# Optimization experiments

Hardware: AMD Instinct MI355X
Metric: run time of the kernel (lower is better)

## Reference

```python
import jax, jax.numpy as jnp
import numpy as np

N, E, D, L = 100000, 500000, 128, 5
NUM_ATOM_FEATS, ATOM_VOCAB = 9, 120
NUM_BOND_FEATS, BOND_VOCAB = 3, 8
BN_EPS = 1e-5


def setup_inputs() -> dict:
    key = jax.random.key(0)
    ks = jax.random.split(key, 16)
    inp = {
        "x": jax.random.randint(ks[0], (N, NUM_ATOM_FEATS), 0, ATOM_VOCAB),
        "edge_index": jax.random.randint(ks[1], (2, E), 0, N),
        "edge_attr": jax.random.randint(ks[2], (E, NUM_BOND_FEATS), 0, BOND_VOCAB),
        "edge_weight": jax.random.uniform(ks[3], (E,), dtype=jnp.float32),
        # parameters
        "atom_emb": jax.random.normal(ks[4], (NUM_ATOM_FEATS, ATOM_VOCAB, D), dtype=jnp.float32) * 0.02,
        "bond_emb": jax.random.normal(ks[5], (L, NUM_BOND_FEATS, BOND_VOCAB, D), dtype=jnp.float32) * 0.02,
        "eps": jnp.zeros((L,), dtype=jnp.float32),
        "W1": jax.random.normal(ks[6], (L, D, 2 * D), dtype=jnp.float32) / np.sqrt(D),
        "b1": jnp.zeros((L, 2 * D), dtype=jnp.float32),
        "g1": jnp.ones((L, 2 * D), dtype=jnp.float32),
        "bt1": jnp.zeros((L, 2 * D), dtype=jnp.float32),
        "W2": jax.random.normal(ks[7], (L, 2 * D, D), dtype=jnp.float32) / np.sqrt(2 * D),
        "b2": jnp.zeros((L, D), dtype=jnp.float32),
        "g_out": jnp.ones((L, D), dtype=jnp.float32),
        "bt_out": jnp.zeros((L, D), dtype=jnp.float32),
    }
    return inp


def _batchnorm(h, g, b):
    # training-mode BN over node axis, biased variance (matches torch BN normalization)
    mu = jnp.mean(h, axis=0)
    var = jnp.mean((h - mu) ** 2, axis=0)
    return g * (h - mu) * jax.lax.rsqrt(var + BN_EPS) + b


def reference(x, edge_index, edge_attr, edge_weight,
              atom_emb, bond_emb, eps, W1, b1, g1, bt1, W2, b2, g_out, bt_out):
    # AtomEncoder: sum per-column embedding lookups -> [N, D]
    h = atom_emb[jnp.arange(NUM_ATOM_FEATS)[None, :], x].sum(axis=1)
    src, dst = edge_index[0], edge_index[1]
    ew = edge_weight[:, None]
    for l in range(L):
        # BondEncoder for layer l -> [E, D]
        e = bond_emb[l][jnp.arange(NUM_BOND_FEATS)[None, :], edge_attr].sum(axis=1)
        # message: relu(x_j + edge_emb) * edge_weight ; aggregate: scatter-add at dst
        m = jax.nn.relu(h[src] + e) * ew
        agg = jax.ops.segment_sum(m, dst, num_segments=N)
        z = (1.0 + eps[l]) * h + agg
        # GIN MLP: Linear -> BN -> ReLU -> Linear
        z = jax.nn.relu(_batchnorm(z @ W1[l] + b1[l], g1[l], bt1[l])) @ W2[l] + b2[l]
        # outer BatchNorm; dropout is identity in eval mode
        h_new = _batchnorm(z, g_out[l], bt_out[l])
        h = h_new if l == L - 1 else jax.nn.relu(h_new)
    return h
```

## Files before the change

### kernel.cpp

```cpp
#include <hip/hip_runtime.h>
#include <hip/hip_bf16.h>
#include <hip/hip_fp16.h>

#define NN 100000
#define EE 500000
#define NP 100096

typedef _Float16 f16;
typedef __attribute__((ext_vector_type(8))) _Float16 f16x8;
typedef __attribute__((ext_vector_type(4))) _Float16 f16x4;
typedef __attribute__((ext_vector_type(4))) float f32x4;

__global__ __launch_bounds__(256) void prep_kernel(const float* __restrict__ W1,
                                                   const float* __restrict__ W2,
                                                   const float* __restrict__ bemb,
                                                   f16* __restrict__ w1f,
                                                   f16* __restrict__ w2f,
                                                   f16* __restrict__ bembf) {
  int gid = blockIdx.x * 256 + threadIdx.x;
  if (gid < 163840) {
    int l = gid / 32768; int rem = gid % 32768;
    int k = rem / 256;   int n = rem % 256;
    int ctg = n >> 4, m = n & 15;
    int c = k >> 5, q = (k >> 3) & 3, e = k & 7;
    int lane = q * 16 + m;
    w1f[l * 32768 + ((ctg * 4 + c) * 64 + lane) * 8 + e] = (f16)W1[gid];
  } else if (gid < 327680) {
    int g = gid - 163840;
    int l = g / 32768; int rem = g % 32768;
    int k = rem / 128; int n = rem % 128;
    int ctg = n >> 4, m = n & 15;
    int c = k >> 5, q = (k >> 3) & 3, e = k & 7;
    int lane = q * 16 + m;
    w2f[l * 32768 + ((ctg * 8 + c) * 64 + lane) * 8 + e] = (f16)W2[g];
  } else if (gid < 343040) {
    int g = gid - 327680;
    bembf[g] = (f16)bemb[g];
  }
}

__global__ __launch_bounds__(256) void zero_deg_kernel(int* __restrict__ deg) {
  int i = blockIdx.x * 256 + threadIdx.x;
  if (i < NN) deg[i] = 0;
}

__global__ __launch_bounds__(256) void hist_kernel(const int* __restrict__ ei, int* __restrict__ deg) {
  int e = blockIdx.x * 256 + threadIdx.x;
  if (e < EE) atomicAdd(&deg[ei[EE + e]], 1);
}

__global__ __launch_bounds__(256) void scan1_kernel(const int* __restrict__ deg,
                                                    int* __restrict__ offs,
                                                    int* __restrict__ bsum) {
  __shared__ int sh[256];
  int b = blockIdx.x, t = threadIdx.x;
  int base = b * 1024 + t * 4;
  int v[4];
  int s = 0;
#pragma unroll
  for (int i = 0; i < 4; ++i) { v[i] = (base + i < NN) ? deg[base + i] : 0; s += v[i]; }
  sh[t] = s;
  __syncthreads();
  for (int off = 1; off < 256; off <<= 1) {
    int x = (t >= off) ? sh[t - off] : 0;
    __syncthreads();
    sh[t] += x;
    __syncthreads();
  }
  int excl = sh[t] - s;
  if (t == 255) bsum[b] = sh[255];
  int run = excl;
#pragma unroll
  for (int i = 0; i < 4; ++i) {
    if (base + i < NN) offs[base + i] = run;
    run += v[i];
  }
}

__global__ void scan2_kernel(int* __restrict__ bsum, int nb) {
  if (threadIdx.x == 0 && blockIdx.x == 0) {
    int run = 0;
    for (int i = 0; i < nb; ++i) { int v = bsum[i]; bsum[i] = run; run += v; }
  }
}

__global__ __launch_bounds__(256) void scan3_kernel(int* __restrict__ offs,
                                                    const int* __restrict__ bsum,
                                                    int* __restrict__ cursor) {
  int i = blockIdx.x * 256 + threadIdx.x;
  if (i < NN) {
    int v = offs[i] + bsum[i >> 10];
    offs[i] = v;
    cursor[i] = v;
  } else if (i == NN) {
    offs[NN] = EE;
  }
}

__global__ __launch_bounds__(256) void scatter_kernel(const int* __restrict__ ei,
                                                      const int* __restrict__ ea,
                                                      const float* __restrict__ ew,
                                                      int* __restrict__ cursor,
                                                      int* __restrict__ pk,
                                                      float* __restrict__ wsrt) {
  int e = blockIdx.x * 256 + threadIdx.x;
  if (e >= EE) return;
  int dst = ei[EE + e];
  int pos = atomicAdd(&cursor[dst], 1);
  int src = ei[e];
  int a0 = ea[e * 3 + 0], a1 = ea[e * 3 + 1], a2 = ea[e * 3 + 2];
  pk[pos] = src | (a0 << 17) | (a1 << 20) | (a2 << 23);
  wsrt[pos] = ew[e];
}

__global__ __launch_bounds__(256) void zero_slices_kernel(float* __restrict__ p) {
  int i = blockIdx.x * 256 + threadIdx.x;
  *(float4*)(p + i * 4) = float4{0.f, 0.f, 0.f, 0.f};
}

__global__ __launch_bounds__(256) void atom_kernel(const int* __restrict__ x,
                                                   const float* __restrict__ aemb,
                                                   f16* __restrict__ hf) {
  int gid = blockIdx.x * 256 + threadIdx.x;
  int n = gid >> 5, qq = gid & 31;
  if (n >= NN) return;
  float4 s = {0.f, 0.f, 0.f, 0.f};
#pragma unroll
  for (int f = 0; f < 9; ++f) {
    int xi = x[n * 9 + f];
    float4 v = *(const float4*)(aemb + (f * 120 + xi) * 128 + qq * 4);
    s.x += v.x; s.y += v.y; s.z += v.z; s.w += v.w;
  }
  f16x4 o;
  o[0] = (f16)s.x; o[1] = (f16)s.y; o[2] = (f16)s.z; o[3] = (f16)s.w;
  *(f16x4*)(hf + (long)n * 128 + qq * 4) = o;
}

__global__ __launch_bounds__(256) void edge_agg_kernel(const int* __restrict__ offs,
                                                       const int* __restrict__ pk,
                                                       const float* __restrict__ wsrt,
                                                       const f16* __restrict__ bembf,
                                                       const float* __restrict__ eps, int l,
                                                       const f16* __restrict__ hf,
                                                       f16* __restrict__ zb) {
  int gid = blockIdx.x * 256 + threadIdx.x;
  int n = gid >> 4, d0 = (gid & 15) * 8;
  if (n >= NN) {
    f16x8 z = {0, 0, 0, 0, 0, 0, 0, 0};
    *(f16x8*)(zb + (long)n * 128 + d0) = z;
    return;
  }
  int s0 = offs[n], s1 = offs[n + 1];
  float e1 = 1.f + eps[l];
  f16x8 hn = *(const f16x8*)(hf + (long)n * 128 + d0);
  float acc[8];
#pragma unroll
  for (int i = 0; i < 8; ++i) acc[i] = e1 * (float)hn[i];
  for (int e = s0; e < s1; ++e) {
    int p = pk[e];
    float w = wsrt[e];
    int src = p & 131071;
    f16x8 b0 = *(const f16x8*)(bembf + (((p >> 17) & 7)) * 128 + d0);
    f16x8 b1 = *(const f16x8*)(bembf + (8 + ((p >> 20) & 7)) * 128 + d0);
    f16x8 b2 = *(const f16x8*)(bembf + (16 + ((p >> 23) & 7)) * 128 + d0);
    f16x8 hs = *(const f16x8*)(hf + (long)src * 128 + d0);
    f16x8 sm = hs + b0 + b1 + b2;
#pragma unroll
    for (int i = 0; i < 8; ++i) {
      float sv = (float)sm[i];
      acc[i] += fmaxf(sv, 0.f) * w;
    }
  }
  f16x8 o;
#pragma unroll
  for (int i = 0; i < 8; ++i) o[i] = (f16)acc[i];
  *(f16x8*)(zb + (long)n * 128 + d0) = o;
}

__global__ __launch_bounds__(256) void gemm1_kernel(const f16* __restrict__ zb,
                                                    const f16* __restrict__ w1f,
                                                    f16* __restrict__ t1f,
                                                    float* __restrict__ sum1s,
                                                    float* __restrict__ sq1s) {
  __shared__ __align__(16) char ldsraw[17408];
  const int tid = threadIdx.x;
  const int lane = tid & 63, w = tid >> 6;
  const int wr = w >> 1, wc = w & 1;
  const int m = lane & 15, q = lane >> 4;
  const int rbase = blockIdx.x * 64;
  const int cb = blockIdx.y;
  const int slice = blockIdx.x & 15;

  f16x8 B[4][4];
#pragma unroll
  for (int ct = 0; ct < 4; ++ct)
#pragma unroll
    for (int c = 0; c < 4; ++c)
      B[ct][c] = *(const f16x8*)(w1f + (((cb * 8 + wc * 4 + ct) * 4 + c) * 64 + lane) * 8);

  {
    f16x8 st[4];
    const int tofs = tid * 16;
#pragma unroll
    for (int j = 0; j < 4; ++j)
      st[j] = *(const f16x8*)(zb + (long)rbase * 128 + (tofs + j * 4096) / 2);
#pragma unroll
    for (int j = 0; j < 4; ++j) {
      int ofs = tofs + j * 4096;
      int row = ofs >> 8, colb = ofs & 255;
      *(f16x8*)(ldsraw + row * 256 + (colb ^ ((row & 7) << 4))) = st[j];
    }
  }
  __syncthreads();

  f16x8 A[2][4];
#pragma unroll
  for (int rt = 0; rt < 2; ++rt) {
    int row = wr * 32 + rt * 16 + m;
    int rs = row * 256, sw = (row & 7) << 4;
#pragma unroll
    for (int c = 0; c < 4; ++c) {
      int colb = c * 64 + q * 16;
      A[rt][c] = *(const f16x8*)(ldsraw + rs + (colb ^ sw));
    }
  }

  f32x4 acc[2][4];
  const f32x4 zf = {0.f, 0.f, 0.f, 0.f};
#pragma unroll
  for (int a = 0; a < 2; ++a)
#pragma unroll
    for (int b = 0; b < 4; ++b) acc[a][b] = zf;

#pragma unroll
  for (int c = 0; c < 4; ++c)
#pragma unroll
    for (int rt = 0; rt < 2; ++rt)
#pragma unroll
      for (int ct = 0; ct < 4; ++ct)
        acc[rt][ct] = __builtin_amdgcn_mfma_f32_16x16x32_f16(A[rt][c], B[ct][c], acc[rt][ct], 0, 0, 0);

  __syncthreads();
  f16 (*sh)[136] = (f16(*)[136])ldsraw;

#pragma unroll
  for (int ct = 0; ct < 4; ++ct) {
    int lc = wc * 64 + ct * 16 + m;
    int gc = cb * 128 + lc;
    float s = 0.f, s2 = 0.f;
#pragma unroll
    for (int rt = 0; rt < 2; ++rt) {
      int lr = wr * 32 + rt * 16 + q * 4;
#pragma unroll
      for (int i = 0; i < 4; ++i) {
        float v = acc[rt][ct][i];
        s += v; s2 += v * v;
        sh[lr + i][lc] = (f16)v;
      }
    }
    s  += __shfl_xor(s, 16);  s  += __shfl_xor(s, 32);
    s2 += __shfl_xor(s2, 16); s2 += __shfl_xor(s2, 32);
    if (q == 0) {
      unsafeAtomicAdd(&sum1s[slice * 256 + gc], s);
      unsafeAtomicAdd(&sq1s[slice * 256 + gc], s2);
    }
  }
  __syncthreads();
  const int colc = tid & 15, r0 = tid >> 4;
#pragma unroll
  for (int j = 0; j < 4; ++j) {
    int r = j * 16 + r0;
    f16x8 v = *(const f16x8*)(&sh[r][colc * 8]);
    *(f16x8*)(t1f + (long)(rbase + r) * 256 + cb * 128 + colc * 8) = v;
  }
}

__global__ void stats_kernel(float* __restrict__ sums, float* __restrict__ sqs,
                             const float* __restrict__ g, const float* __restrict__ bt,
                             float* __restrict__ scale, float* __restrict__ shift, int C) {
  int j = blockIdx.x * blockDim.x + threadIdx.x;
  if (j >= C) return;
  float s = 0.f, s2 = 0.f;
#pragma unroll
  for (int k = 0; k < 16; ++k) {
    s += sums[k * C + j]; s2 += sqs[k * C + j];
    sums[k * C + j] = 0.f; sqs[k * C + j] = 0.f;
  }
  float mu = s * (1.f / NN);
  float var = s2 * (1.f / NN) - mu * mu;
  var = fmaxf(var, 0.f);
  float is = rsqrtf(var + 1e-5f);
  float sc = g[j] * is;
  scale[j] = sc;
  shift[j] = bt[j] - mu * sc;
}

__global__ __launch_bounds__(256) void gemm2_kernel(const f16* __restrict__ a1,
                                                    const f16* __restrict__ w2f,
                                                    const float* __restrict__ scale1,
                                                    const float* __restrict__ shift1,
                                                    f16* __restrict__ zb,
                                                    float* __restrict__ sum2s,
                                                    float* __restrict__ sq2s) {
  __shared__ __align__(16) char ldsraw[32768];
  const int tid = threadIdx.x;
  const int lane = tid & 63, w = tid >> 6;
  const int wr = w >> 1, wc = w & 1;
  const int m = lane & 15, q = lane >> 4;
  const int rbase = blockIdx.x * 64;
  const int slice = blockIdx.x & 15;

  {
    f16x8 st[8];
    const int tofs = tid * 16;
#pragma unroll
    for (int j = 0; j < 8; ++j)
      st[j] = *(const f16x8*)(a1 + (long)rbase * 256 + (tofs + j * 4096) / 2);
#pragma unroll
    for (int j = 0; j < 8; ++j) {
      int ofs = tofs + j * 4096;
      int row = ofs >> 9, colb = ofs & 511;
      int k0 = colb >> 1;
      float4 sa = *(const float4*)(scale1 + k0);
      float4 sb = *(const float4*)(scale1 + k0 + 4);
      float4 ha = *(const float4*)(shift1 + k0);
      float4 hb = *(const float4*)(shift1 + k0 + 4);
      f16x8 u = st[j], o;
      o[0] = (f16)fmaxf((float)u[0] * sa.x + ha.x, 0.f);
      o[1] = (f16)fmaxf((float)u[1] * sa.y + ha.y, 0.f);
      o[2] = (f16)fmaxf((float)u[2] * sa.z + ha.z, 0.f);
      o[3] = (f16)fmaxf((float)u[3] * sa.w + ha.w, 0.f);
      o[4] = (f16)fmaxf((float)u[4] * sb.x + hb.x, 0.f);
      o[5] = (f16)fmaxf((float)u[5] * sb.y + hb.y, 0.f);
      o[6] = (f16)fmaxf((float)u[6] * sb.z + hb.z, 0.f);
      o[7] = (f16)fmaxf((float)u[7] * sb.w + hb.w, 0.f);
      *(f16x8*)(ldsraw + row * 512 + (colb ^ ((row & 7) << 4))) = o;
    }
  }
  __syncthreads();

  f32x4 acc[2][4];
  const f32x4 zf = {0.f, 0.f, 0.f, 0.f};
#pragma unroll
  for (int a = 0; a < 2; ++a)
#pragma unroll
    for (int b = 0; b < 4; ++b) acc[a][b] = zf;

#pragma unroll
  for (int hh = 0; hh < 2; ++hh) {
    f16x8 A[2][4], B[4][4];
#pragma unroll
    for (int rt = 0; rt < 2; ++rt) {
      int row = wr * 32 + rt * 16 + m;
      int rs = row * 512, sw = (row & 7) << 4;
#pragma unroll
      for (int c = 0; c < 4; ++c) {
        int colb = (hh * 4 + c) * 64 + q * 16;
        A[rt][c] = *(const f16x8*)(ldsraw + rs + (colb ^ sw));
      }
    }
#pragma unroll
    for (int ct = 0; ct < 4; ++ct)
#pragma unroll
      for (int c = 0; c < 4; ++c)
        B[ct][c] = *(const f16x8*)(w2f + (((wc * 4 + ct) * 8 + hh * 4 + c) * 64 + lane) * 8);
#pragma unroll
    for (int c = 0; c < 4; ++c)
#pragma unroll
      for (int rt = 0; rt < 2; ++rt)
#pragma unroll
        for (int ct = 0; ct < 4; ++ct)
          acc[rt][ct] = __builtin_amdgcn_mfma_f32_16x16x32_f16(A[rt][c], B[ct][c], acc[rt][ct], 0, 0, 0);
  }

  __syncthreads();
  f16 (*sh)[136] = (f16(*)[136])ldsraw;

#pragma unroll
  for (int ct = 0; ct < 4; ++ct) {
    int gc = wc * 64 + ct * 16 + m;
    float s = 0.f, s2 = 0.f;
#pragma unroll
    for (int rt = 0; rt < 2; ++rt) {
      int grow = rbase + wr * 32 + rt * 16 + q * 4;
      int lr = wr * 32 + rt * 16 + q * 4;
#pragma unroll
      for (int i = 0; i < 4; ++i) {
        float v = acc[rt][ct][i];
        float vv = (grow + i < NN) ? v : 0.f;
        s += vv; s2 += vv * vv;
        sh[lr + i][gc] = (f16)v;
      }
    }
    s  += __shfl_xor(s, 16);  s  += __shfl_xor(s, 32);
    s2 += __shfl_xor(s2, 16); s2 += __shfl_xor(s2, 32);
    if (q == 0) {
      unsafeAtomicAdd(&sum2s[slice * 128 + gc], s);
      unsafeAtomicAdd(&sq2s[slice * 128 + gc], s2);
    }
  }
  __syncthreads();
  const int colc = tid & 15, r0 = tid >> 4;
#pragma unroll
  for (int j = 0; j < 4; ++j) {
    int r = j * 16 + r0;
    f16x8 v = *(const f16x8*)(&sh[r][colc * 8]);
    *(f16x8*)(zb + (long)(rbase + r) * 128 + colc * 8) = v;
  }
}

__global__ __launch_bounds__(256) void apply_kernel(const f16* __restrict__ zb,
                                                    const float* __restrict__ scale2,
                                                    const float* __restrict__ shift2,
                                                    int last,
                                                    f16* __restrict__ hf,
                                                    float* __restrict__ outp) {
  int gid = blockIdx.x * 256 + threadIdx.x;
  int n = gid >> 5, qq = gid & 31;
  if (n >= NN) return;
  f16x4 u = *(const f16x4*)(zb + (long)n * 128 + qq * 4);
  float4 sc = *(const float4*)(scale2 + qq * 4);
  float4 sh = *(const float4*)(shift2 + qq * 4);
  float y0 = (float)u[0] * sc.x + sh.x;
  float y1 = (float)u[1] * sc.y + sh.y;
  float y2 = (float)u[2] * sc.z + sh.z;
  float y3 = (float)u[3] * sc.w + sh.w;
  if (last) {
    float4 o = {y0, y1, y2, y3};
    *(float4*)(outp + (long)n * 128 + qq * 4) = o;
  } else {
    f16x4 o;
    o[0] = (f16)fmaxf(y0, 0.f); o[1] = (f16)fmaxf(y1, 0.f);
    o[2] = (f16)fmaxf(y2, 0.f); o[3] = (f16)fmaxf(y3, 0.f);
    *(f16x4*)(hf + (long)n * 128 + qq * 4) = o;
  }
}

extern "C" void kernel_launch(void* const* d_in, const int* in_sizes, int n_in,
                              void* d_out, int out_size, void* d_ws, size_t ws_size,
                              hipStream_t stream) {
  (void)in_sizes; (void)n_in; (void)out_size; (void)ws_size;
  const int*   x      = (const int*)d_in[0];
  const int*   ei     = (const int*)d_in[1];
  const int*   ea     = (const int*)d_in[2];
  const float* ew     = (const float*)d_in[3];
  const float* aemb   = (const float*)d_in[4];
  const float* bemb   = (const float*)d_in[5];
  const float* eps    = (const float*)d_in[6];
  const float* W1     = (const float*)d_in[7];
  const float* g1     = (const float*)d_in[9];
  const float* bt1    = (const float*)d_in[10];
  const float* W2     = (const float*)d_in[11];
  const float* g_out  = (const float*)d_in[13];
  const float* bt_out = (const float*)d_in[14];

  float* outp = (float*)d_out;

  char* ws = (char*)d_ws;
  f16*   hf    = (f16*)(ws);
  f16*   zb    = (f16*)(ws + 25624576);
  f16*   t1f   = (f16*)(ws + 51249152);
  f16*   w1f   = (f16*)(ws + 102498304);
  f16*   w2f   = (f16*)(ws + 102825984);
  f16*   bembf = (f16*)(ws + 103153664);
  float* ssbuf = (float*)(ws + 103184384);
  float* slices= (float*)(ws + 103187456);
  int*   deg    = (int*)(ws + 103236608);
  int*   offs   = (int*)(ws + 103636608);
  int*   cursor = (int*)(ws + 104036624);
  int*   bsum   = (int*)(ws + 104436624);
  int*   pk     = (int*)(ws + 104437024);
  float* wsrt   = (float*)(ws + 106437024);

  float* scale1 = ssbuf;        float* shift1 = ssbuf + 256;
  float* scale2 = ssbuf + 512;  float* shift2 = ssbuf + 640;
  float* sum1s = slices;
  float* sq1s  = slices + 4096;
  float* sum2s = slices + 8192;
  float* sq2s  = slices + 10240;

  prep_kernel<<<1340, 256, 0, stream>>>(W1, W2, bemb, w1f, w2f, bembf);
  zero_deg_kernel<<<391, 256, 0, stream>>>(deg);
  hist_kernel<<<1954, 256, 0, stream>>>(ei, deg);
  scan1_kernel<<<98, 256, 0, stream>>>(deg, offs, bsum);
  scan2_kernel<<<1, 64, 0, stream>>>(bsum, 98);
  scan3_kernel<<<392, 256, 0, stream>>>(offs, bsum, cursor);
  scatter_kernel<<<1954, 256, 0, stream>>>(ei, ea, ew, cursor, pk, wsrt);
  zero_slices_kernel<<<12, 256, 0, stream>>>(slices);
  atom_kernel<<<12500, 256, 0, stream>>>(x, aemb, hf);

  for (int l = 0; l < 5; ++l) {
    edge_agg_kernel<<<6256, 256, 0, stream>>>(offs, pk, wsrt, bembf + l * 3072, eps, l, hf, zb);
    gemm1_kernel<<<dim3(1564, 2), 256, 0, stream>>>(zb, w1f + l * 32768, t1f, sum1s, sq1s);
    stats_kernel<<<1, 256, 0, stream>>>(sum1s, sq1s, g1 + l * 256, bt1 + l * 256, scale1, shift1, 256);
    gemm2_kernel<<<1564, 256, 0, stream>>>(t1f, w2f + l * 32768, scale1, shift1, zb, sum2s, sq2s);
    stats_kernel<<<1, 128, 0, stream>>>(sum2s, sq2s, g_out + l * 128, bt_out + l * 128, scale2, shift2, 128);
    apply_kernel<<<12500, 256, 0, stream>>>(zb, scale2, shift2, (l == 4) ? 1 : 0, hf, outp);
  }
}
```

Before: 673.5 us.

## Fuse BN stats and outer BN apply into neighbouring kernels, drop stats launches

Removes the separate stats kernels and the per-layer apply kernel. Each consumer block now recomputes the BN scale and shift from the per-slice sums. The outer BN plus ReLU of the previous layer is applied on the fly inside the edge aggregation, to both self and neighbour features. Stat-slice zeroing moves into the first block of later kernels, which relies on stream ordering between launches. This saves a full read/write pass over node features and ten or more launches per layer set, at the cost of extra per-edge FMAs and redundant stat reductions in every block.

```diff
diff --git a/kernel.cpp b/kernel.cpp
--- a/kernel.cpp
+++ b/kernel.cpp
@@ -140,7 +140,7 @@
                                                        const int* __restrict__ pk,
                                                        const float* __restrict__ wsrt,
                                                        const f16* __restrict__ bembf,
-                                                       const float* __restrict__ eps, int l,
+                                                       const float* __restrict__ eps,
                                                        const f16* __restrict__ hf,
                                                        f16* __restrict__ zb) {
   int gid = blockIdx.x * 256 + threadIdx.x;
@@ -151,7 +151,7 @@
     return;
   }
   int s0 = offs[n], s1 = offs[n + 1];
-  float e1 = 1.f + eps[l];
+  float e1 = 1.f + eps[0];
   f16x8 hn = *(const f16x8*)(hf + (long)n * 128 + d0);
   float acc[8];
 #pragma unroll
@@ -177,11 +177,83 @@
   *(f16x8*)(zb + (long)n * 128 + d0) = o;
 }
 
+__global__ __launch_bounds__(256) void edge_agg_bn_kernel(const int* __restrict__ offs,
+                                                          const int* __restrict__ pk,
+                                                          const float* __restrict__ wsrt,
+                                                          const f16* __restrict__ bembf,
+                                                          const float* __restrict__ eps, int l,
+                                                          const f16* __restrict__ t2,
+                                                          const float* __restrict__ sum2s,
+                                                          const float* __restrict__ sq2s,
+                                                          const float* __restrict__ g2,
+                                                          const float* __restrict__ bt2,
+                                                          float* __restrict__ s1z,
+                                                          f16* __restrict__ zb) {
+  __shared__ float sc2[128], sh2[128];
+  const int tid = threadIdx.x;
+  if (tid < 128) {
+    float s = 0.f, s2 = 0.f;
+#pragma unroll
+    for (int k = 0; k < 16; ++k) { s += sum2s[k * 128 + tid]; s2 += sq2s[k * 128 + tid]; }
+    float mu = s * (1.f / NN);
+    float var = fmaxf(s2 * (1.f / NN) - mu * mu, 0.f);
+    float is = rsqrtf(var + 1e-5f);
+    float sc = g2[tid] * is;
+    sc2[tid] = sc;
+    sh2[tid] = bt2[tid] - mu * sc;
+  }
+  if (blockIdx.x == 0) {
+#pragma unroll
+    for (int j = 0; j < 8; ++j)
+      *(float4*)(s1z + (j * 256 + tid) * 4) = float4{0.f, 0.f, 0.f, 0.f};
+  }
+  __syncthreads();
+  int gid = blockIdx.x * 256 + tid;
+  int n = gid >> 4, d0 = (gid & 15) * 8;
+  if (n >= NN) {
+    f16x8 z = {0, 0, 0, 0, 0, 0, 0, 0};
+    *(f16x8*)(zb + (long)n * 128 + d0) = z;
+    return;
+  }
+  float4 svA = *(const float4*)(sc2 + d0), svB = *(const float4*)(sc2 + d0 + 4);
+  float4 shA = *(const float4*)(sh2 + d0), shB = *(const float4*)(sh2 + d0 + 4);
+  float sv[8] = {svA.x, svA.y, svA.z, svA.w, svB.x, svB.y, svB.z, svB.w};
+  float hv[8] = {shA.x, shA.y, shA.z, shA.w, shB.x, shB.y, shB.z, shB.w};
+  int s0 = offs[n], s1 = offs[n + 1];
+  float e1 = 1.f + eps[l];
+  f16x8 hn = *(const f16x8*)(t2 + (long)n * 128 + d0);
+  float acc[8];
+#pragma unroll
+  for (int i = 0; i < 8; ++i)
+    acc[i] = e1 * fmaxf((float)hn[i] * sv[i] + hv[i], 0.f);
+  for (int e = s0; e < s1; ++e) {
+    int p = pk[e];
+    float w = wsrt[e];
+    int src = p & 131071;
+    f16x8 b0 = *(const f16x8*)(bembf + (((p >> 17) & 7)) * 128 + d0);
+    f16x8 b1 = *(const f16x8*)(bembf + (8 + ((p >> 20) & 7)) * 128 + d0);
+    f16x8 b2 = *(const f16x8*)(bembf + (16 + ((p >> 23) & 7)) * 128 + d0);
+    f16x8 hs = *(const f16x8*)(t2 + (long)src * 128 + d0);
+    f16x8 bs = b0 + b1 + b2;
+#pragma unroll
+    for (int i = 0; i < 8; ++i) {
+      float y = fmaxf((float)hs[i] * sv[i] + hv[i], 0.f);
+      float s = y + (float)bs[i];
+      acc[i] += fmaxf(s, 0.f) * w;
+    }
+  }
+  f16x8 o;
+#pragma unroll
+  for (int i = 0; i < 8; ++i) o[i] = (f16)acc[i];
+  *(f16x8*)(zb + (long)n * 128 + d0) = o;
+}
+
 __global__ __launch_bounds__(256) void gemm1_kernel(const f16* __restrict__ zb,
                                                     const f16* __restrict__ w1f,
                                                     f16* __restrict__ t1f,
                                                     float* __restrict__ sum1s,
-                                                    float* __restrict__ sq1s) {
+                                                    float* __restrict__ sq1s,
+                                                    float* __restrict__ s2z) {
   __shared__ __align__(16) char ldsraw[17408];
   const int tid = threadIdx.x;
   const int lane = tid & 63, w = tid >> 6;
@@ -191,6 +263,12 @@
   const int cb = blockIdx.y;
   const int slice = blockIdx.x & 15;
 
+  if (blockIdx.x == 0 && cb == 0) {
+#pragma unroll
+    for (int j = 0; j < 4; ++j)
+      *(float4*)(s2z + (j * 256 + tid) * 4) = float4{0.f, 0.f, 0.f, 0.f};
+  }
+
   f16x8 B[4][4];
 #pragma unroll
   for (int ct = 0; ct < 4; ++ct)
@@ -275,34 +353,18 @@
   }
 }
 
-__global__ void stats_kernel(float* __restrict__ sums, float* __restrict__ sqs,
-                             const float* __restrict__ g, const float* __restrict__ bt,
-                             float* __restrict__ scale, float* __restrict__ shift, int C) {
-  int j = blockIdx.x * blockDim.x + threadIdx.x;
-  if (j >= C) return;
-  float s = 0.f, s2 = 0.f;
-#pragma unroll
-  for (int k = 0; k < 16; ++k) {
-    s += sums[k * C + j]; s2 += sqs[k * C + j];
-    sums[k * C + j] = 0.f; sqs[k * C + j] = 0.f;
-  }
-  float mu = s * (1.f / NN);
-  float var = s2 * (1.f / NN) - mu * mu;
-  var = fmaxf(var, 0.f);
-  float is = rsqrtf(var + 1e-5f);
-  float sc = g[j] * is;
-  scale[j] = sc;
-  shift[j] = bt[j] - mu * sc;
-}
-
 __global__ __launch_bounds__(256) void gemm2_kernel(const f16* __restrict__ a1,
                                                     const f16* __restrict__ w2f,
-                                                    const float* __restrict__ scale1,
-                                                    const float* __restrict__ shift1,
-                                                    f16* __restrict__ zb,
+                                                    const float* __restrict__ sum1s,
+                                                    const float* __restrict__ sq1s,
+                                                    const float* __restrict__ g1,
+                                                    const float* __restrict__ bt1,
+                                                    f16* __restrict__ t2out,
                                                     float* __restrict__ sum2s,
                                                     float* __restrict__ sq2s) {
-  __shared__ __align__(16) char ldsraw[32768];
+  __shared__ __align__(16) char ldsraw[34816];
+  float* sc1 = (float*)(ldsraw + 32768);
+  float* sh1 = (float*)(ldsraw + 33792);
   const int tid = threadIdx.x;
   const int lane = tid & 63, w = tid >> 6;
   const int wr = w >> 1, wc = w & 1;
@@ -310,21 +372,35 @@
   const int rbase = blockIdx.x * 64;
   const int slice = blockIdx.x & 15;
 
+  f16x8 st[8];
+  const int tofs = tid * 16;
+#pragma unroll
+  for (int j = 0; j < 8; ++j)
+    st[j] = *(const f16x8*)(a1 + (long)rbase * 256 + (tofs + j * 4096) / 2);
+
   {
-    f16x8 st[8];
-    const int tofs = tid * 16;
-#pragma unroll
-    for (int j = 0; j < 8; ++j)
-      st[j] = *(const f16x8*)(a1 + (long)rbase * 256 + (tofs + j * 4096) / 2);
+    float s = 0.f, s2 = 0.f;
+#pragma unroll
+    for (int k = 0; k < 16; ++k) { s += sum1s[k * 256 + tid]; s2 += sq1s[k * 256 + tid]; }
+    float mu = s * (1.f / NN);
+    float var = fmaxf(s2 * (1.f / NN) - mu * mu, 0.f);
+    float is = rsqrtf(var + 1e-5f);
+    float sc = g1[tid] * is;
+    sc1[tid] = sc;
+    sh1[tid] = bt1[tid] - mu * sc;
+  }
+  __syncthreads();
+
+  {
+    const int k0 = (tid & 31) * 8;
+    float4 sa = *(const float4*)(sc1 + k0);
+    float4 sb = *(const float4*)(sc1 + k0 + 4);
+    float4 ha = *(const float4*)(sh1 + k0);
+    float4 hb = *(const float4*)(sh1 + k0 + 4);
 #pragma unroll
     for (int j = 0; j < 8; ++j) {
       int ofs = tofs + j * 4096;
       int row = ofs >> 9, colb = ofs & 511;
-      int k0 = colb >> 1;
-      float4 sa = *(const float4*)(scale1 + k0);
-      float4 sb = *(const float4*)(scale1 + k0 + 4);
-      float4 ha = *(const float4*)(shift1 + k0);
-      float4 hb = *(const float4*)(shift1 + k0 + 4);
       f16x8 u = st[j], o;
       o[0] = (f16)fmaxf((float)u[0] * sa.x + ha.x, 0.f);
       o[1] = (f16)fmaxf((float)u[1] * sa.y + ha.y, 0.f);
@@ -405,34 +481,48 @@
   for (int j = 0; j < 4; ++j) {
     int r = j * 16 + r0;
     f16x8 v = *(const f16x8*)(&sh[r][colc * 8]);
-    *(f16x8*)(zb + (long)(rbase + r) * 128 + colc * 8) = v;
-  }
-}
-
-__global__ __launch_bounds__(256) void apply_kernel(const f16* __restrict__ zb,
-                                                    const float* __restrict__ scale2,
-                                                    const float* __restrict__ shift2,
-                                                    int last,
-                                                    f16* __restrict__ hf,
+    *(f16x8*)(t2out + (long)(rbase + r) * 128 + colc * 8) = v;
+  }
+}
+
+__global__ __launch_bounds__(256) void apply_kernel(const f16* __restrict__ t2,
+                                                    const float* __restrict__ sum2s,
+                                                    const float* __restrict__ sq2s,
+                                                    const float* __restrict__ g2,
+                                                    const float* __restrict__ bt2,
                                                     float* __restrict__ outp) {
-  int gid = blockIdx.x * 256 + threadIdx.x;
-  int n = gid >> 5, qq = gid & 31;
-  if (n >= NN) return;
-  f16x4 u = *(const f16x4*)(zb + (long)n * 128 + qq * 4);
-  float4 sc = *(const float4*)(scale2 + qq * 4);
-  float4 sh = *(const float4*)(shift2 + qq * 4);
-  float y0 = (float)u[0] * sc.x + sh.x;
-  float y1 = (float)u[1] * sc.y + sh.y;
-  float y2 = (float)u[2] * sc.z + sh.z;
-  float y3 = (float)u[3] * sc.w + sh.w;
-  if (last) {
-    float4 o = {y0, y1, y2, y3};
-    *(float4*)(outp + (long)n * 128 + qq * 4) = o;
-  } else {
-    f16x4 o;
-    o[0] = (f16)fmaxf(y0, 0.f); o[1] = (f16)fmaxf(y1, 0.f);
-    o[2] = (f16)fmaxf(y2, 0.f); o[3] = (f16)fmaxf(y3, 0.f);
-    *(f16x4*)(hf + (long)n * 128 + qq * 4) = o;
+  __shared__ float sc2[128], sh2[128];
+  const int tid = threadIdx.x;
+  if (tid < 128) {
+    float s = 0.f, s2 = 0.f;
+#pragma unroll
+    for (int k = 0; k < 16; ++k) { s += sum2s[k * 128 + tid]; s2 += sq2s[k * 128 + tid]; }
+    float mu = s * (1.f / NN);
+    float var = fmaxf(s2 * (1.f / NN) - mu * mu, 0.f);
+    float is = rsqrtf(var + 1e-5f);
+    float sc = g2[tid] * is;
+    sc2[tid] = sc;
+    sh2[tid] = bt2[tid] - mu * sc;
+  }
+  __syncthreads();
+  const int rbase = blockIdx.x * 64;
+#pragma unroll
+  for (int k = 0; k < 4; ++k) {
+    int ci = tid + k * 256;
+    int r = ci >> 4, c8 = ci & 15;
+    int row = rbase + r;
+    if (row >= NN) continue;
+    f16x8 u = *(const f16x8*)(t2 + (long)row * 128 + c8 * 8);
+    float4 sa = *(const float4*)(sc2 + c8 * 8);
+    float4 sb = *(const float4*)(sc2 + c8 * 8 + 4);
+    float4 ha = *(const float4*)(sh2 + c8 * 8);
+    float4 hb = *(const float4*)(sh2 + c8 * 8 + 4);
+    float4 o0 = {(float)u[0] * sa.x + ha.x, (float)u[1] * sa.y + ha.y,
+                 (float)u[2] * sa.z + ha.z, (float)u[3] * sa.w + ha.w};
+    float4 o1 = {(float)u[4] * sb.x + hb.x, (float)u[5] * sb.y + hb.y,
+                 (float)u[6] * sb.z + hb.z, (float)u[7] * sb.w + hb.w};
+    *(float4*)(outp + (long)row * 128 + c8 * 8) = o0;
+    *(float4*)(outp + (long)row * 128 + c8 * 8 + 4) = o1;
   }
 }
 
@@ -463,7 +553,6 @@
   f16*   w1f   = (f16*)(ws + 102498304);
   f16*   w2f   = (f16*)(ws + 102825984);
   f16*   bembf = (f16*)(ws + 103153664);
-  float* ssbuf = (float*)(ws + 103184384);
   float* slices= (float*)(ws + 103187456);
   int*   deg    = (int*)(ws + 103236608);
   int*   offs   = (int*)(ws + 103636608);
@@ -472,8 +561,6 @@
   int*   pk     = (int*)(ws + 104437024);
   float* wsrt   = (float*)(ws + 106437024);
 
-  float* scale1 = ssbuf;        float* shift1 = ssbuf + 256;
-  float* scale2 = ssbuf + 512;  float* shift2 = ssbuf + 640;
   float* sum1s = slices;
   float* sq1s  = slices + 4096;
   float* sum2s = slices + 8192;
@@ -490,11 +577,18 @@
   atom_kernel<<<12500, 256, 0, stream>>>(x, aemb, hf);
 
   for (int l = 0; l < 5; ++l) {
-    edge_agg_kernel<<<6256, 256, 0, stream>>>(offs, pk, wsrt, bembf + l * 3072, eps, l, hf, zb);
-    gemm1_kernel<<<dim3(1564, 2), 256, 0, stream>>>(zb, w1f + l * 32768, t1f, sum1s, sq1s);
-    stats_kernel<<<1, 256, 0, stream>>>(sum1s, sq1s, g1 + l * 256, bt1 + l * 256, scale1, shift1, 256);
-    gemm2_kernel<<<1564, 256, 0, stream>>>(t1f, w2f + l * 32768, scale1, shift1, zb, sum2s, sq2s);
-    stats_kernel<<<1, 128, 0, stream>>>(sum2s, sq2s, g_out + l * 128, bt_out + l * 128, scale2, shift2, 128);
-    apply_kernel<<<12500, 256, 0, stream>>>(zb, scale2, shift2, (l == 4) ? 1 : 0, hf, outp);
-  }
-}
+    if (l == 0) {
+      edge_agg_kernel<<<6256, 256, 0, stream>>>(offs, pk, wsrt, bembf, eps, hf, zb);
+    } else {
+      edge_agg_bn_kernel<<<6256, 256, 0, stream>>>(offs, pk, wsrt, bembf + l * 3072, eps, l,
+                                                   hf, sum2s, sq2s,
+                                                   g_out + (l - 1) * 128, bt_out + (l - 1) * 128,
+                                                   sum1s, zb);
+    }
+    gemm1_kernel<<<dim3(1564, 2), 256, 0, stream>>>(zb, w1f + l * 32768, t1f, sum1s, sq1s, sum2s);
+    gemm2_kernel<<<1564, 256, 0, stream>>>(t1f, w2f + l * 32768, sum1s, sq1s,
+                                           g1 + l * 256, bt1 + l * 256, hf, sum2s, sq2s);
+    if (l == 4)
+      apply_kernel<<<1564, 256, 0, stream>>>(hf, sum2s, sq2s, g_out + 512, bt_out + 512, outp);
+  }
+}
```

Result: faster. 626.8 us (-6.9%).
